# Optimization experiments

Hardware: AMD Instinct MI355X
Metric: run time of the kernel (lower is better)

The kernel has to match this reference:

```python
import jax, jax.numpy as jnp
import numpy as np

B = 8192
NUM_NODES = 100000
EMB = 128
W1D, W2D, W3D = 64, 128, 256   # witness_dims
CODE = 128
HID = 64                        # hardcoded hidden_dim in WitnessExtractor / decoder
TOTW = W1D + W2D + W3D          # 448


def _linear_params(key, fan_in, fan_out):
    k1, k2 = jax.random.split(key)
    bound = 1.0 / np.sqrt(fan_in)
    w = jax.random.uniform(k1, (fan_out, fan_in), jnp.float32, -bound, bound)
    b = jax.random.uniform(k2, (fan_out,), jnp.float32, -bound, bound)
    return w, b


def setup_inputs() -> dict:
    key = jax.random.key(0)
    ks = jax.random.split(key, 12)
    u = jax.random.randint(ks[0], (B,), 0, NUM_NODES, dtype=jnp.int64 if jax.config.jax_enable_x64 else jnp.int32)
    v = jax.random.randint(ks[1], (B,), 0, NUM_NODES, dtype=u.dtype)
    emb = jax.random.normal(ks[2], (NUM_NODES, EMB), jnp.float32)
    e1_w1, e1_b1 = _linear_params(ks[3], 2 * EMB, HID)
    e1_w2, e1_b2 = _linear_params(ks[4], HID, W1D)
    e2_w1, e2_b1 = _linear_params(ks[5], 2 * EMB + W1D, HID)
    e2_w2, e2_b2 = _linear_params(ks[6], HID, W2D)
    e3_w1, e3_b1 = _linear_params(ks[7], 2 * EMB + W2D, HID)
    e3_w2, e3_b2 = _linear_params(ks[8], HID, W3D)
    trop_w = jax.random.normal(ks[9], (CODE, TOTW), jnp.float32)  # init_scale=1.0
    dec_w1, dec_b1 = _linear_params(ks[10], CODE, HID)
    dec_w2, dec_b2 = _linear_params(ks[11], HID, 1)
    return dict(u=u, v=v, emb=emb,
                e1_w1=e1_w1, e1_b1=e1_b1, e1_w2=e1_w2, e1_b2=e1_b2,
                e2_w1=e2_w1, e2_b1=e2_b1, e2_w2=e2_w2, e2_b2=e2_b2,
                e3_w1=e3_w1, e3_b1=e3_b1, e3_w2=e3_w2, e3_b2=e3_b2,
                trop_w=trop_w, dec_w1=dec_w1, dec_b1=dec_b1,
                dec_w2=dec_w2, dec_b2=dec_b2)


def _witness(x, w1, b1, w2, b2):
    h = jax.nn.relu(x @ w1.T + b1)
    return jax.nn.sigmoid(h @ w2.T + b2)


def reference(u, v, emb,
              e1_w1, e1_b1, e1_w2, e1_b2,
              e2_w1, e2_b1, e2_w2, e2_b2,
              e3_w1, e3_b1, e3_w2, e3_b2,
              trop_w, dec_w1, dec_b1, dec_w2, dec_b2):
    u_emb = emb[u]                               # [B, EMB]
    v_emb = emb[v]
    base = jnp.concatenate([u_emb, v_emb], axis=1)  # [B, 2*EMB]
    w1 = _witness(base, e1_w1, e1_b1, e1_w2, e1_b2)
    w2 = _witness(jnp.concatenate([base, w1], axis=1), e2_w1, e2_b1, e2_w2, e2_b2)
    w3 = _witness(jnp.concatenate([base, w2], axis=1), e3_w1, e3_b1, e3_w2, e3_b2)
    wit = jnp.concatenate([w1, w2, w3], axis=1)  # [B, TOTW]
    # tropical (min-plus) matmul: code[b,o] = min_j (wit[b,j] + trop_w[o,j])
    code = jnp.min(wit[:, None, :] + trop_w[None, :, :], axis=2)  # [B, CODE]
    h = jax.nn.relu(code @ dec_w1.T + dec_b1)
    return h @ dec_w2.T + dec_b2                 # [B, 1]
```

## Files before the change

### kernel.cpp

```cpp
#include <hip/hip_runtime.h>
#include <hip/hip_fp16.h>
#include <math.h>

#define BATCH 8192
#define EMB 128
#define TILE 16
#define NTHREADS 1024
#define NWAVES 16
#define CH 136
#define WITS 450
#define SLOT 32
#define PBS 17

#define OFF_E1W1 0
#define OFF_E1W2 16384
#define OFF_E2W1 20480
#define OFF_E2W2 40960
#define OFF_E3W1 49152
#define OFF_E3W2 73728
#define OFF_DW1  90112
#define OFF_DW2  98304
#define W_DENSE  98368

typedef __attribute__((ext_vector_type(8))) _Float16 v8h;
typedef __attribute__((ext_vector_type(4))) float v4f;

struct Smem {
    _Float16 XB[32 * CH];
    _Float16 W12C[24 * CH];
    _Float16 H[8 * CH];
    _Float16 CODE[16 * CH];
    _Float16 WITrm[TILE * WITS];
    float PB0[64 * PBS];
    float PB1[64 * PBS];
    unsigned int ent[128 * SLOT];
    unsigned int cnt[128];
};

__global__ __launch_bounds__(1024) void prep_kernel(
    const float* __restrict__ s0, const float* __restrict__ s1,
    const float* __restrict__ s2, const float* __restrict__ s3,
    const float* __restrict__ s4, const float* __restrict__ s5,
    const float* __restrict__ s6, const float* __restrict__ s7,
    const float* __restrict__ trop, _Float16* __restrict__ ws)
{
    const int b = blockIdx.x;
    const int tid = threadIdx.x;
    if (b < 25) {
        const int idx4 = (b * 1024 + tid) * 4;
        if (idx4 >= W_DENSE) return;
        const float* src; int off;
        if      (idx4 < OFF_E1W2) { src = s0; off = OFF_E1W1; }
        else if (idx4 < OFF_E2W1) { src = s1; off = OFF_E1W2; }
        else if (idx4 < OFF_E2W2) { src = s2; off = OFF_E2W1; }
        else if (idx4 < OFF_E3W1) { src = s3; off = OFF_E2W2; }
        else if (idx4 < OFF_E3W2) { src = s4; off = OFF_E3W1; }
        else if (idx4 < OFF_DW1)  { src = s5; off = OFF_E3W2; }
        else if (idx4 < OFF_DW2)  { src = s6; off = OFF_DW1;  }
        else                      { src = s7; off = OFF_DW2;  }
        const float4 v = *(const float4*)(src + (idx4 - off));
        _Float16* dst = ws + idx4;
        dst[0] = (_Float16)v.x; dst[1] = (_Float16)v.y;
        dst[2] = (_Float16)v.z; dst[3] = (_Float16)v.w;
    } else {
        const int lane = tid & 63;
        const int wave = tid >> 6;
        const int o = (b - 25) * 16 + wave;
        if (o >= 128) return;
        unsigned int* base = (unsigned int*)(ws + W_DENSE);

        const float* row = trop + (size_t)o * 448;
        float vals[7];
        float mn = 1e30f;
        #pragma unroll
        for (int it = 0; it < 7; ++it) {
            vals[it] = row[lane + it * 64];
            mn = fminf(mn, vals[it]);
        }
        mn = fminf(mn, __shfl_xor(mn, 1, 64));
        mn = fminf(mn, __shfl_xor(mn, 2, 64));
        mn = fminf(mn, __shfl_xor(mn, 4, 64));
        mn = fminf(mn, __shfl_xor(mn, 8, 64));
        mn = fminf(mn, __shfl_xor(mn, 16, 64));
        mn = fminf(mn, __shfl_xor(mn, 32, 64));
        const float thr = mn + 1.02f;

        const unsigned long long ltmask = (1ull << lane) - 1ull;
        unsigned int pos0 = 0;
        #pragma unroll
        for (int it = 0; it < 7; ++it) {
            const bool sel = vals[it] <= thr;
            const unsigned long long m = __ballot(sel);
            if (sel) {
                const unsigned int pos = pos0 + (unsigned)__popcll(m & ltmask);
                if (pos < SLOT) {
                    const unsigned short hb =
                        __builtin_bit_cast(unsigned short, (_Float16)vals[it]);
                    base[o * SLOT + pos] = ((unsigned)(lane + it * 64) << 16) | hb;
                }
            }
            pos0 += (unsigned)__popcll(m);
        }
        if (lane == 0) base[4096 + o] = pos0;
    }
}

template <int K, int STEPS0, int O, int ACT, bool CHUNKW, bool RMW>
__device__ __forceinline__ void dense_mfma(
    const _Float16* __restrict__ Wg, const float* __restrict__ bias,
    const _Float16* A0, const _Float16* A1,
    _Float16* OutC, _Float16* OutRM, int rmbase, int wave, int lane)
{
    constexpr int STEPS = K / 32;
    static_assert(STEPS % 2 == 0, "even steps");
    constexpr int NJOBS = O / 16;
    const int l15 = lane & 15;
    const int quad = lane >> 4;

    for (int nt = wave; nt < NJOBS; nt += NWAVES) {
        v4f c0 = {0.f, 0.f, 0.f, 0.f};
        v4f c1 = {0.f, 0.f, 0.f, 0.f};
        const _Float16* wrow = Wg + (size_t)(nt * 16 + l15) * K + quad * 8;
        #pragma unroll
        for (int s = 0; s < STEPS; s += 2) {
            const int g0 = s * 4 + quad;
            const int g1 = (s + 1) * 4 + quad;
            const _Float16* a0p = (s < STEPS0)
                ? (A0 + g0 * CH + l15 * 8)
                : (A1 + (g0 - STEPS0 * 4) * CH + l15 * 8);
            const _Float16* a1p = ((s + 1) < STEPS0)
                ? (A0 + g1 * CH + l15 * 8)
                : (A1 + (g1 - STEPS0 * 4) * CH + l15 * 8);
            const v8h a0 = *(const v8h*)a0p;
            const v8h b0 = *(const v8h*)(wrow + s * 32);
            const v8h a1 = *(const v8h*)a1p;
            const v8h b1 = *(const v8h*)(wrow + (s + 1) * 32);
            c0 = __builtin_amdgcn_mfma_f32_16x16x32_f16(a0, b0, c0, 0, 0, 0);
            c1 = __builtin_amdgcn_mfma_f32_16x16x32_f16(a1, b1, c1, 0, 0, 0);
        }
        const v4f c = c0 + c1;
        const int o = nt * 16 + l15;
        const float bs = bias[o];
        #pragma unroll
        for (int i = 0; i < 4; ++i) {
            float vv = c[i] + bs;
            if (ACT == 0) vv = fmaxf(vv, 0.f);
            else          vv = 1.f / (1.f + __expf(-vv));
            const int m = quad * 4 + i;
            const _Float16 hv = (_Float16)vv;
            if (CHUNKW) OutC[(o >> 3) * CH + m * 8 + (o & 7)] = hv;
            if (RMW)    OutRM[m * WITS + rmbase + o] = hv;
        }
    }
}

__device__ __forceinline__ void stage_base3(
    const _Float16* __restrict__ ws,
    const float* __restrict__ b1, const float* __restrict__ b2,
    const float* __restrict__ b3,
    const _Float16* XB, _Float16* H, float* PB0, float* PB1,
    int wave, int lane)
{
    if (wave >= 12) return;
    const int tgt = wave >> 2;
    const int nt  = wave & 3;
    const int l15 = lane & 15;
    const int quad = lane >> 4;
    const int o = nt * 16 + l15;
    const _Float16* wrow;
    const float* bias;
    if (tgt == 0)      { wrow = ws + OFF_E1W1 + (size_t)o * 256; bias = b1; }
    else if (tgt == 1) { wrow = ws + OFF_E2W1 + (size_t)o * 320; bias = b2; }
    else               { wrow = ws + OFF_E3W1 + (size_t)o * 384; bias = b3; }
    wrow += quad * 8;
    v4f c0 = {0.f, 0.f, 0.f, 0.f};
    v4f c1 = {0.f, 0.f, 0.f, 0.f};
    #pragma unroll
    for (int s = 0; s < 8; s += 2) {
        const v8h a0 = *(const v8h*)(XB + (s * 4 + quad) * CH + l15 * 8);
        const v8h b0 = *(const v8h*)(wrow + s * 32);
        const v8h a1 = *(const v8h*)(XB + ((s + 1) * 4 + quad) * CH + l15 * 8);
        const v8h b1v = *(const v8h*)(wrow + (s + 1) * 32);
        c0 = __builtin_amdgcn_mfma_f32_16x16x32_f16(a0, b0, c0, 0, 0, 0);
        c1 = __builtin_amdgcn_mfma_f32_16x16x32_f16(a1, b1v, c1, 0, 0, 0);
    }
    const v4f c = c0 + c1;
    const float bs = bias[o];
    if (tgt == 0) {
        #pragma unroll
        for (int i = 0; i < 4; ++i) {
            const float vv = fmaxf(c[i] + bs, 0.f);
            const int m = quad * 4 + i;
            H[(o >> 3) * CH + m * 8 + (o & 7)] = (_Float16)vv;
        }
    } else {
        float* PB = (tgt == 1) ? PB0 : PB1;
        #pragma unroll
        for (int i = 0; i < 4; ++i)
            PB[o * PBS + quad * 4 + i] = c[i] + bs;
    }
}

template <int KW, int RS>
__device__ __forceinline__ void dense_addpb(
    const _Float16* __restrict__ Wg,
    const _Float16* A0, const float* __restrict__ PB,
    _Float16* OutH, int wave, int lane)
{
    constexpr int STEPS = KW / 32;
    static_assert(STEPS % 2 == 0, "even steps");
    if (wave >= 4) return;
    const int l15 = lane & 15;
    const int quad = lane >> 4;
    const int o = wave * 16 + l15;
    const _Float16* wrow = Wg + (size_t)o * RS + quad * 8;
    v4f c0, c1 = {0.f, 0.f, 0.f, 0.f};
    #pragma unroll
    for (int i = 0; i < 4; ++i) c0[i] = PB[o * PBS + quad * 4 + i];
    #pragma unroll
    for (int s = 0; s < STEPS; s += 2) {
        const v8h a0 = *(const v8h*)(A0 + (s * 4 + quad) * CH + l15 * 8);
        const v8h b0 = *(const v8h*)(wrow + s * 32);
        const v8h a1 = *(const v8h*)(A0 + ((s + 1) * 4 + quad) * CH + l15 * 8);
        const v8h b1 = *(const v8h*)(wrow + (s + 1) * 32);
        c0 = __builtin_amdgcn_mfma_f32_16x16x32_f16(a0, b0, c0, 0, 0, 0);
        c1 = __builtin_amdgcn_mfma_f32_16x16x32_f16(a1, b1, c1, 0, 0, 0);
    }
    const v4f c = c0 + c1;
    #pragma unroll
    for (int i = 0; i < 4; ++i) {
        const float vv = fmaxf(c[i], 0.f);
        const int m = quad * 4 + i;
        OutH[(o >> 3) * CH + m * 8 + (o & 7)] = (_Float16)vv;
    }
}

__global__ __launch_bounds__(NTHREADS, 8) void tacit_fused_kernel(
    const int* __restrict__ u, const int* __restrict__ v,
    const float* __restrict__ emb,
    const float* __restrict__ e1_b1, const float* __restrict__ e1_b2,
    const float* __restrict__ e2_b1, const float* __restrict__ e2_b2,
    const float* __restrict__ e3_b1, const float* __restrict__ e3_b2,
    const float* __restrict__ dec_b1, const float* __restrict__ dec_b2,
    const float* __restrict__ trop,
    const _Float16* __restrict__ ws,
    float* __restrict__ out)
{
    __shared__ Smem S;
    const int tid = threadIdx.x;
    const int lane = tid & 63;
    const int wave = tid >> 6;
    const int row0 = blockIdx.x * TILE;

    {
        const unsigned int* base = (const unsigned int*)(ws + W_DENSE);
        *(uint4*)&S.ent[tid * 4] = *(const uint4*)(base + tid * 4);
        if (tid < 32) *(uint4*)&S.cnt[tid * 4] = *(const uint4*)(base + 4096 + tid * 4);
    }
    if (tid < 512) {
        const int row = tid & 15;
        const int kq = tid >> 4;
        const int node = (kq < 16) ? u[row0 + row] : v[row0 + row];
        const int col = (kq & 15) * 8;
        const float4 f0 = *(const float4*)(emb + (size_t)node * EMB + col);
        const float4 f1 = *(const float4*)(emb + (size_t)node * EMB + col + 4);
        v8h hv;
        hv[0] = (_Float16)f0.x; hv[1] = (_Float16)f0.y;
        hv[2] = (_Float16)f0.z; hv[3] = (_Float16)f0.w;
        hv[4] = (_Float16)f1.x; hv[5] = (_Float16)f1.y;
        hv[6] = (_Float16)f1.z; hv[7] = (_Float16)f1.w;
        *(v8h*)&S.XB[kq * CH + row * 8] = hv;
    }
    __syncthreads();

    stage_base3(ws, e1_b1, e2_b1, e3_b1, S.XB, S.H, S.PB0, S.PB1, wave, lane);
    __syncthreads();

    dense_mfma<64, 2, 64, 1, true, true>(ws + OFF_E1W2, e1_b2, S.H, nullptr,
                                         S.W12C, S.WITrm, 0, wave, lane);
    __syncthreads();

    dense_addpb<64, 320>(ws + OFF_E2W1 + 256, S.W12C, S.PB0, S.H, wave, lane);
    __syncthreads();

    dense_mfma<64, 2, 128, 1, true, true>(ws + OFF_E2W2, e2_b2, S.H, nullptr,
                                          S.W12C + 8 * CH, S.WITrm, 64, wave, lane);
    __syncthreads();

    dense_addpb<128, 384>(ws + OFF_E3W1 + 256, S.W12C + 8 * CH, S.PB1, S.H, wave, lane);
    __syncthreads();

    dense_mfma<64, 2, 256, 1, false, true>(ws + OFF_E3W2, e3_b2, S.H, nullptr,
                                           nullptr, S.WITrm, 192, wave, lane);
    __syncthreads();

    {
        const int r = lane & 15;
        const int cp = lane >> 4;
        const _Float16* wrow = &S.WITrm[r * WITS];
        float acc[8];
        int idx[8], end8[8];
        #pragma unroll
        for (int i = 0; i < 8; ++i) {
            const int o = (wave << 3) + i;
            const int n = (int)S.cnt[o];
            idx[i] = o * SLOT + cp;
            end8[i] = o * SLOT + (n < SLOT ? n : SLOT);
            acc[i] = 1e30f;
        }
        bool any = true;
        while (any) {
            any = false;
            #pragma unroll
            for (int i = 0; i < 8; ++i) {
                if (idx[i] < end8[i]) {
                    const unsigned int cwv = S.ent[idx[i]];
                    const int j = (int)(cwv >> 16);
                    const float tv = (float)__builtin_bit_cast(
                        _Float16, (unsigned short)(cwv & 0xffffu));
                    acc[i] = fminf(acc[i], (float)wrow[j] + tv);
                    idx[i] += 4;
                    any = true;
                }
            }
        }
        #pragma unroll
        for (int i = 0; i < 8; ++i) {
            const int o = (wave << 3) + i;
            if ((int)S.cnt[o] > SLOT) {
                const float* trow = trop + (size_t)o * 448;
                for (int j = cp; j < 448; j += 4)
                    acc[i] = fminf(acc[i], (float)wrow[j] + trow[j]);
            }
        }
        #pragma unroll
        for (int i = 0; i < 8; ++i) {
            float a = acc[i];
            a = fminf(a, __shfl_xor(a, 16, 64));
            a = fminf(a, __shfl_xor(a, 32, 64));
            if (cp == 0) {
                const int o = (wave << 3) + i;
                S.CODE[(o >> 3) * CH + r * 8 + (o & 7)] = (_Float16)a;
            }
        }
    }
    __syncthreads();

    dense_mfma<128, 4, 64, 0, true, false>(ws + OFF_DW1, dec_b1, S.CODE, nullptr,
                                           S.H, nullptr, 0, wave, lane);
    __syncthreads();

    if (tid < 64) {
        const int r = lane & 15;
        const int part = lane >> 4;
        const _Float16* w2 = ws + OFF_DW2;
        float s = 0.f;
        #pragma unroll
        for (int q = 0; q < 2; ++q) {
            const int c = part + q * 4;
            const v8h hr = *(const v8h*)(&S.H[c * CH + r * 8]);
            const v8h wr = *(const v8h*)(w2 + c * 8);
            #pragma unroll
            for (int t = 0; t < 8; ++t) s += (float)hr[t] * (float)wr[t];
        }
        s += __shfl_xor(s, 16, 64);
        s += __shfl_xor(s, 32, 64);
        if (part == 0) out[row0 + r] = s + dec_b2[0];
    }
}

extern "C" void kernel_launch(void* const* d_in, const int* in_sizes, int n_in,
                              void* d_out, int out_size, void* d_ws, size_t ws_size,
                              hipStream_t stream) {
    const int*   u      = (const int*)d_in[0];
    const int*   v      = (const int*)d_in[1];
    const float* emb    = (const float*)d_in[2];
    const float* e1_w1  = (const float*)d_in[3];
    const float* e1_b1  = (const float*)d_in[4];
    const float* e1_w2  = (const float*)d_in[5];
    const float* e1_b2  = (const float*)d_in[6];
    const float* e2_w1  = (const float*)d_in[7];
    const float* e2_b1  = (const float*)d_in[8];
    const float* e2_w2  = (const float*)d_in[9];
    const float* e2_b2  = (const float*)d_in[10];
    const float* e3_w1  = (const float*)d_in[11];
    const float* e3_b1  = (const float*)d_in[12];
    const float* e3_w2  = (const float*)d_in[13];
    const float* e3_b2  = (const float*)d_in[14];
    const float* trop_w = (const float*)d_in[15];
    const float* dec_w1 = (const float*)d_in[16];
    const float* dec_b1 = (const float*)d_in[17];
    const float* dec_w2 = (const float*)d_in[18];
    const float* dec_b2 = (const float*)d_in[19];
    float* out = (float*)d_out;
    _Float16* ws = (_Float16*)d_ws;

    prep_kernel<<<33, 1024, 0, stream>>>(
        e1_w1, e1_w2, e2_w1, e2_w2, e3_w1, e3_w2, dec_w1, dec_w2, trop_w, ws);

    tacit_fused_kernel<<<BATCH / TILE, NTHREADS, 0, stream>>>(
        u, v, emb,
        e1_b1, e1_b2, e2_b1, e2_b2, e3_b1, e3_b2, dec_b1, dec_b2,
        trop_w, ws, out);
}
```

Baseline: 150.7 us.

## Keep witness partials in registers and unify witness storage in chunked layout

The partial pre-activations for the second and third witness first layers now stay in per-wave registers (hold) instead of going through float shared-memory buffers. Because of that, the waves that computed each partial must run the matching follow-up layer, so the wave-to-job mapping for the stages changes. The separate row-major witness copy is dropped, and all three witnesses are written once into a single chunked buffer. The tropical min-plus stage then reads from that chunked buffer with computed indices. This cuts shared-memory traffic and footprint, which may raise occupancy, at the cost of more complex index math in the gather loop.

New measurement: 151.5 us. Within noise of the previous version (+0.6%).

```diff
diff --git a/kernel.cpp b/kernel.cpp
--- a/kernel.cpp
+++ b/kernel.cpp
@@ -8,9 +8,7 @@
 #define NTHREADS 1024
 #define NWAVES 16
 #define CH 136
-#define WITS 450
 #define SLOT 32
-#define PBS 17
 
 #define OFF_E1W1 0
 #define OFF_E1W2 16384
@@ -27,12 +25,9 @@
 
 struct Smem {
     _Float16 XB[32 * CH];
-    _Float16 W12C[24 * CH];
+    _Float16 WC[56 * CH];
     _Float16 H[8 * CH];
     _Float16 CODE[16 * CH];
-    _Float16 WITrm[TILE * WITS];
-    float PB0[64 * PBS];
-    float PB1[64 * PBS];
     unsigned int ent[128 * SLOT];
     unsigned int cnt[128];
 };
@@ -105,118 +100,53 @@
     }
 }
 
-template <int K, int STEPS0, int O, int ACT, bool CHUNKW, bool RMW>
-__device__ __forceinline__ void dense_mfma(
+template <int K, int O, int ACT>
+__device__ __forceinline__ void dense_job(
     const _Float16* __restrict__ Wg, const float* __restrict__ bias,
-    const _Float16* A0, const _Float16* A1,
-    _Float16* OutC, _Float16* OutRM, int rmbase, int wave, int lane)
+    const _Float16* A0, _Float16* OutC, int jid, int lane)
 {
     constexpr int STEPS = K / 32;
     static_assert(STEPS % 2 == 0, "even steps");
-    constexpr int NJOBS = O / 16;
     const int l15 = lane & 15;
     const int quad = lane >> 4;
-
-    for (int nt = wave; nt < NJOBS; nt += NWAVES) {
-        v4f c0 = {0.f, 0.f, 0.f, 0.f};
-        v4f c1 = {0.f, 0.f, 0.f, 0.f};
-        const _Float16* wrow = Wg + (size_t)(nt * 16 + l15) * K + quad * 8;
-        #pragma unroll
-        for (int s = 0; s < STEPS; s += 2) {
-            const int g0 = s * 4 + quad;
-            const int g1 = (s + 1) * 4 + quad;
-            const _Float16* a0p = (s < STEPS0)
-                ? (A0 + g0 * CH + l15 * 8)
-                : (A1 + (g0 - STEPS0 * 4) * CH + l15 * 8);
-            const _Float16* a1p = ((s + 1) < STEPS0)
-                ? (A0 + g1 * CH + l15 * 8)
-                : (A1 + (g1 - STEPS0 * 4) * CH + l15 * 8);
-            const v8h a0 = *(const v8h*)a0p;
-            const v8h b0 = *(const v8h*)(wrow + s * 32);
-            const v8h a1 = *(const v8h*)a1p;
-            const v8h b1 = *(const v8h*)(wrow + (s + 1) * 32);
-            c0 = __builtin_amdgcn_mfma_f32_16x16x32_f16(a0, b0, c0, 0, 0, 0);
-            c1 = __builtin_amdgcn_mfma_f32_16x16x32_f16(a1, b1, c1, 0, 0, 0);
-        }
-        const v4f c = c0 + c1;
-        const int o = nt * 16 + l15;
-        const float bs = bias[o];
-        #pragma unroll
-        for (int i = 0; i < 4; ++i) {
-            float vv = c[i] + bs;
-            if (ACT == 0) vv = fmaxf(vv, 0.f);
-            else          vv = 1.f / (1.f + __expf(-vv));
-            const int m = quad * 4 + i;
-            const _Float16 hv = (_Float16)vv;
-            if (CHUNKW) OutC[(o >> 3) * CH + m * 8 + (o & 7)] = hv;
-            if (RMW)    OutRM[m * WITS + rmbase + o] = hv;
-        }
-    }
-}
-
-__device__ __forceinline__ void stage_base3(
-    const _Float16* __restrict__ ws,
-    const float* __restrict__ b1, const float* __restrict__ b2,
-    const float* __restrict__ b3,
-    const _Float16* XB, _Float16* H, float* PB0, float* PB1,
-    int wave, int lane)
-{
-    if (wave >= 12) return;
-    const int tgt = wave >> 2;
-    const int nt  = wave & 3;
-    const int l15 = lane & 15;
-    const int quad = lane >> 4;
-    const int o = nt * 16 + l15;
-    const _Float16* wrow;
-    const float* bias;
-    if (tgt == 0)      { wrow = ws + OFF_E1W1 + (size_t)o * 256; bias = b1; }
-    else if (tgt == 1) { wrow = ws + OFF_E2W1 + (size_t)o * 320; bias = b2; }
-    else               { wrow = ws + OFF_E3W1 + (size_t)o * 384; bias = b3; }
-    wrow += quad * 8;
+    const int o = jid * 16 + l15;
+    const _Float16* wrow = Wg + (size_t)o * K + quad * 8;
     v4f c0 = {0.f, 0.f, 0.f, 0.f};
     v4f c1 = {0.f, 0.f, 0.f, 0.f};
     #pragma unroll
-    for (int s = 0; s < 8; s += 2) {
-        const v8h a0 = *(const v8h*)(XB + (s * 4 + quad) * CH + l15 * 8);
+    for (int s = 0; s < STEPS; s += 2) {
+        const v8h a0 = *(const v8h*)(A0 + (s * 4 + quad) * CH + l15 * 8);
         const v8h b0 = *(const v8h*)(wrow + s * 32);
-        const v8h a1 = *(const v8h*)(XB + ((s + 1) * 4 + quad) * CH + l15 * 8);
-        const v8h b1v = *(const v8h*)(wrow + (s + 1) * 32);
+        const v8h a1 = *(const v8h*)(A0 + ((s + 1) * 4 + quad) * CH + l15 * 8);
+        const v8h b1 = *(const v8h*)(wrow + (s + 1) * 32);
         c0 = __builtin_amdgcn_mfma_f32_16x16x32_f16(a0, b0, c0, 0, 0, 0);
-        c1 = __builtin_amdgcn_mfma_f32_16x16x32_f16(a1, b1v, c1, 0, 0, 0);
+        c1 = __builtin_amdgcn_mfma_f32_16x16x32_f16(a1, b1, c1, 0, 0, 0);
     }
     const v4f c = c0 + c1;
     const float bs = bias[o];
-    if (tgt == 0) {
-        #pragma unroll
-        for (int i = 0; i < 4; ++i) {
-            const float vv = fmaxf(c[i] + bs, 0.f);
-            const int m = quad * 4 + i;
-            H[(o >> 3) * CH + m * 8 + (o & 7)] = (_Float16)vv;
-        }
-    } else {
-        float* PB = (tgt == 1) ? PB0 : PB1;
-        #pragma unroll
-        for (int i = 0; i < 4; ++i)
-            PB[o * PBS + quad * 4 + i] = c[i] + bs;
+    #pragma unroll
+    for (int i = 0; i < 4; ++i) {
+        float vv = c[i] + bs;
+        if (ACT == 0) vv = fmaxf(vv, 0.f);
+        else          vv = 1.f / (1.f + __expf(-vv));
+        const int m = quad * 4 + i;
+        OutC[(o >> 3) * CH + m * 8 + (o & 7)] = (_Float16)vv;
     }
 }
 
 template <int KW, int RS>
-__device__ __forceinline__ void dense_addpb(
-    const _Float16* __restrict__ Wg,
-    const _Float16* A0, const float* __restrict__ PB,
-    _Float16* OutH, int wave, int lane)
+__device__ __forceinline__ void addpb_job(
+    const _Float16* __restrict__ Wg, const _Float16* A0,
+    const v4f hold, _Float16* OutH, int jid, int lane)
 {
     constexpr int STEPS = KW / 32;
     static_assert(STEPS % 2 == 0, "even steps");
-    if (wave >= 4) return;
     const int l15 = lane & 15;
     const int quad = lane >> 4;
-    const int o = wave * 16 + l15;
+    const int o = jid * 16 + l15;
     const _Float16* wrow = Wg + (size_t)o * RS + quad * 8;
-    v4f c0, c1 = {0.f, 0.f, 0.f, 0.f};
-    #pragma unroll
-    for (int i = 0; i < 4; ++i) c0[i] = PB[o * PBS + quad * 4 + i];
+    v4f c0 = hold;
+    v4f c1 = {0.f, 0.f, 0.f, 0.f};
     #pragma unroll
     for (int s = 0; s < STEPS; s += 2) {
         const v8h a0 = *(const v8h*)(A0 + (s * 4 + quad) * CH + l15 * 8);
@@ -273,31 +203,71 @@
     }
     __syncthreads();
 
-    stage_base3(ws, e1_b1, e2_b1, e3_b1, S.XB, S.H, S.PB0, S.PB1, wave, lane);
-    __syncthreads();
-
-    dense_mfma<64, 2, 64, 1, true, true>(ws + OFF_E1W2, e1_b2, S.H, nullptr,
-                                         S.W12C, S.WITrm, 0, wave, lane);
-    __syncthreads();
-
-    dense_addpb<64, 320>(ws + OFF_E2W1 + 256, S.W12C, S.PB0, S.H, wave, lane);
-    __syncthreads();
-
-    dense_mfma<64, 2, 128, 1, true, true>(ws + OFF_E2W2, e2_b2, S.H, nullptr,
-                                          S.W12C + 8 * CH, S.WITrm, 64, wave, lane);
-    __syncthreads();
-
-    dense_addpb<128, 384>(ws + OFF_E3W1 + 256, S.W12C + 8 * CH, S.PB1, S.H, wave, lane);
-    __syncthreads();
-
-    dense_mfma<64, 2, 256, 1, false, true>(ws + OFF_E3W2, e3_b2, S.H, nullptr,
-                                           nullptr, S.WITrm, 192, wave, lane);
+    v4f hold = {0.f, 0.f, 0.f, 0.f};
+    if (wave < 12) {
+        const int tgt = wave >> 2;
+        const int nt  = wave & 3;
+        const int l15 = lane & 15;
+        const int quad = lane >> 4;
+        const int o = nt * 16 + l15;
+        const _Float16* wrow;
+        const float* bias;
+        if (tgt == 0)      { wrow = ws + OFF_E1W1 + (size_t)o * 256; bias = e1_b1; }
+        else if (tgt == 1) { wrow = ws + OFF_E2W1 + (size_t)o * 320; bias = e2_b1; }
+        else               { wrow = ws + OFF_E3W1 + (size_t)o * 384; bias = e3_b1; }
+        wrow += quad * 8;
+        v4f c0 = {0.f, 0.f, 0.f, 0.f};
+        v4f c1 = {0.f, 0.f, 0.f, 0.f};
+        #pragma unroll
+        for (int s = 0; s < 8; s += 2) {
+            const v8h a0 = *(const v8h*)(S.XB + (s * 4 + quad) * CH + l15 * 8);
+            const v8h b0 = *(const v8h*)(wrow + s * 32);
+            const v8h a1 = *(const v8h*)(S.XB + ((s + 1) * 4 + quad) * CH + l15 * 8);
+            const v8h b1v = *(const v8h*)(wrow + (s + 1) * 32);
+            c0 = __builtin_amdgcn_mfma_f32_16x16x32_f16(a0, b0, c0, 0, 0, 0);
+            c1 = __builtin_amdgcn_mfma_f32_16x16x32_f16(a1, b1v, c1, 0, 0, 0);
+        }
+        const v4f c = c0 + c1;
+        const float bs = bias[o];
+        if (tgt == 0) {
+            #pragma unroll
+            for (int i = 0; i < 4; ++i) {
+                const float vv = fmaxf(c[i] + bs, 0.f);
+                S.H[(o >> 3) * CH + (quad * 4 + i) * 8 + (o & 7)] = (_Float16)vv;
+            }
+        } else {
+            #pragma unroll
+            for (int i = 0; i < 4; ++i) hold[i] = c[i] + bs;
+        }
+    }
+    __syncthreads();
+
+    if (wave < 4)
+        dense_job<64, 64, 1>(ws + OFF_E1W2, e1_b2, S.H, S.WC, wave, lane);
+    __syncthreads();
+
+    if (wave >= 4 && wave < 8)
+        addpb_job<64, 320>(ws + OFF_E2W1 + 256, S.WC, hold, S.H, wave - 4, lane);
+    __syncthreads();
+
+    {
+        const int dnt = (wave < 4) ? wave : (wave >= 12 ? wave - 8 : -1);
+        if (dnt >= 0)
+            dense_job<64, 128, 1>(ws + OFF_E2W2, e2_b2, S.H, S.WC + 8 * CH, dnt, lane);
+    }
+    __syncthreads();
+
+    if (wave >= 8 && wave < 12)
+        addpb_job<128, 384>(ws + OFF_E3W1 + 256, S.WC + 8 * CH, hold, S.H, wave - 8, lane);
+    __syncthreads();
+
+    dense_job<64, 256, 1>(ws + OFF_E3W2, e3_b2, S.H, S.WC + 24 * CH, wave, lane);
     __syncthreads();
 
     {
         const int r = lane & 15;
         const int cp = lane >> 4;
-        const _Float16* wrow = &S.WITrm[r * WITS];
+        const _Float16* wr8 = &S.WC[r * 8];
         float acc[8];
         int idx[8], end8[8];
         #pragma unroll
@@ -318,7 +288,7 @@
                     const int j = (int)(cwv >> 16);
                     const float tv = (float)__builtin_bit_cast(
                         _Float16, (unsigned short)(cwv & 0xffffu));
-                    acc[i] = fminf(acc[i], (float)wrow[j] + tv);
+                    acc[i] = fminf(acc[i], (float)wr8[(j >> 3) * CH + (j & 7)] + tv);
                     idx[i] += 4;
                     any = true;
                 }
@@ -330,7 +300,7 @@
             if ((int)S.cnt[o] > SLOT) {
                 const float* trow = trop + (size_t)o * 448;
                 for (int j = cp; j < 448; j += 4)
-                    acc[i] = fminf(acc[i], (float)wrow[j] + trow[j]);
+                    acc[i] = fminf(acc[i], (float)wr8[(j >> 3) * CH + (j & 7)] + trow[j]);
             }
         }
         #pragma unroll
@@ -346,8 +316,8 @@
     }
     __syncthreads();
 
-    dense_mfma<128, 4, 64, 0, true, false>(ws + OFF_DW1, dec_b1, S.CODE, nullptr,
-                                           S.H, nullptr, 0, wave, lane);
+    if (wave < 4)
+        dense_job<128, 64, 0>(ws + OFF_DW1, dec_b1, S.CODE, S.H, wave, lane);
     __syncthreads();
 
     if (tid < 64) {
```
